# Kernel tuning notes

Measured on AMD Instinct MI355X. Metric: run time of the kernel, lower is better.

## Reference

```python
import jax, jax.numpy as jnp
import numpy as np

B, I, O = 512, 1024, 1024

def setup_inputs() -> dict:
    key = jax.random.key(0)
    kx, kw = jax.random.split(key)
    x = jax.random.normal(kx, (B, I), dtype=jnp.float32)
    W = jax.random.normal(kw, (O, I), dtype=jnp.float32)
    return {"x": x, "W": W}

def reference(x, W):
    # Tropical (max-plus) linear map: y[b, o] = max_i (x[b, i] + W[o, i])
    # Faithful to the torch broadcast-add + max-reduce formulation.
    out = x[..., None, :] + W[None, :, :]  # [B, O, I]
    return jnp.max(out, axis=-1)           # [B, O]
```

## Files before the change

### kernel.cpp

```cpp
#include <hip/hip_runtime.h>


#define B_DIM 512
#define I_DIM 1024
#define O_DIM 1024
#define BT 32
#define OT 64
#define KT 64
#define NCHUNK (I_DIM / KT)
#define XS (BT + 1)
#define WS (OT + 1)

__global__ __launch_bounds__(256, 1) void TropicalLinear_kernel(
    const float* __restrict__ x, const float* __restrict__ W,
    float* __restrict__ y)
{
    __shared__ float xs[KT * XS];
    __shared__ float ws[KT * WS];

    const int tid = threadIdx.x;
    const int to  = tid & 15;
    const int tb  = tid >> 4;
    const int b0  = blockIdx.y * BT;
    const int o0  = blockIdx.x * OT;

    const float4* xg = (const float4*)x;
    const float4* wg = (const float4*)W;

    float4 xr[2];
    float4 wr[4];

    #pragma unroll
    for (int s = 0; s < 2; ++s) {
        const int f = tid + 256 * s;
        const int r = f >> 4, c4 = f & 15;
        xr[s] = xg[(b0 + r) * (I_DIM / 4) + c4];
    }
    #pragma unroll
    for (int s = 0; s < 4; ++s) {
        const int f = tid + 256 * s;
        const int r = f >> 4, c4 = f & 15;
        wr[s] = wg[(o0 + r) * (I_DIM / 4) + c4];
    }

    float acc[2][4];
    #pragma unroll
    for (int i = 0; i < 2; ++i)
        #pragma unroll
        for (int j = 0; j < 4; ++j)
            acc[i][j] = -3.402823466e38f;

    for (int kc = 0; kc < NCHUNK; ++kc) {
        __syncthreads();

        #pragma unroll
        for (int s = 0; s < 2; ++s) {
            const int f = tid + 256 * s;
            const int r = f >> 4, c4 = f & 15;
            xs[(4 * c4 + 0) * XS + r] = xr[s].x;
            xs[(4 * c4 + 1) * XS + r] = xr[s].y;
            xs[(4 * c4 + 2) * XS + r] = xr[s].z;
            xs[(4 * c4 + 3) * XS + r] = xr[s].w;
        }
        #pragma unroll
        for (int s = 0; s < 4; ++s) {
            const int f = tid + 256 * s;
            const int r = f >> 4, c4 = f & 15;
            ws[(4 * c4 + 0) * WS + r] = wr[s].x;
            ws[(4 * c4 + 1) * WS + r] = wr[s].y;
            ws[(4 * c4 + 2) * WS + r] = wr[s].z;
            ws[(4 * c4 + 3) * WS + r] = wr[s].w;
        }
        __syncthreads();

        if (kc + 1 < NCHUNK) {
            const int k4 = (kc + 1) * (KT / 4);
            #pragma unroll
            for (int s = 0; s < 2; ++s) {
                const int f = tid + 256 * s;
                const int r = f >> 4, c4 = f & 15;
                xr[s] = xg[(b0 + r) * (I_DIM / 4) + k4 + c4];
            }
            #pragma unroll
            for (int s = 0; s < 4; ++s) {
                const int f = tid + 256 * s;
                const int r = f >> 4, c4 = f & 15;
                wr[s] = wg[(o0 + r) * (I_DIM / 4) + k4 + c4];
            }
        }

        #pragma unroll 4
        for (int k = 0; k < KT; k += 2) {
            float xa[2], xb[2];
            xa[0] = xs[k * XS + tb];
            xa[1] = xs[k * XS + tb + 16];
            xb[0] = xs[(k + 1) * XS + tb];
            xb[1] = xs[(k + 1) * XS + tb + 16];
            float w0[4], w1[4];
            #pragma unroll
            for (int j = 0; j < 4; ++j) {
                w0[j] = ws[k * WS + 4 * to + j];
                w1[j] = ws[(k + 1) * WS + 4 * to + j];
            }
            #pragma unroll
            for (int i = 0; i < 2; ++i)
                #pragma unroll
                for (int j = 0; j < 4; ++j) {
                    const float s0 = xa[i] + w0[j];
                    const float s1 = xb[i] + w1[j];
                    acc[i][j] = fmaxf(acc[i][j], fmaxf(s0, s1));
                }
        }
    }

    #pragma unroll
    for (int i = 0; i < 2; ++i) {
        float4 v = make_float4(acc[i][0], acc[i][1], acc[i][2], acc[i][3]);
        *(float4*)&y[(b0 + tb + 16 * i) * O_DIM + o0 + 4 * to] = v;
    }
}

extern "C" void kernel_launch(void* const* d_in, const int* in_sizes, int n_in,
                              void* d_out, int out_size, void* d_ws, size_t ws_size,
                              hipStream_t stream) {
    const float* x = (const float*)d_in[0];
    const float* W = (const float*)d_in[1];
    float* y = (float*)d_out;
    dim3 grid(O_DIM / OT, B_DIM / BT);
    dim3 block(256);
    TropicalLinear_kernel<<<grid, block, 0, stream>>>(x, W, y);
}
```

Measured before the change: 106.4 us.

## Use split-K 128x128 tiles with async LDS loads and atomic max reduction

Pre-transposes x and W into workspace so that K-major rows can be streamed straight into LDS with global_load_lds, double-buffered. Each thread now holds an 8x8 register tile of a 128x128 output block, which raises arithmetic per LDS read. The K dimension is split 8 ways to fill the GPU, and partial maxima are merged with int/uint atomic max/min on an output pre-filled with 0xFF. In exchange it adds two transpose launches, a memset and about four million atomics.

```diff
diff --git a/kernel.cpp b/kernel.cpp
--- a/kernel.cpp
+++ b/kernel.cpp
@@ -1,123 +1,136 @@
 #include <hip/hip_runtime.h>
+#include <float.h>
 
 
 #define B_DIM 512
 #define I_DIM 1024
 #define O_DIM 1024
-#define BT 32
-#define OT 64
-#define KT 64
-#define NCHUNK (I_DIM / KT)
-#define XS (BT + 1)
-#define WS (OT + 1)
 
-__global__ __launch_bounds__(256, 1) void TropicalLinear_kernel(
-    const float* __restrict__ x, const float* __restrict__ W,
+#define BT 128
+#define OT 128
+#define KSPLIT 8
+#define KB (I_DIM / KSPLIT)
+#define KT 32
+#define NCH (KB / KT)
+
+__device__ __forceinline__ void g2lds16(const float* g, float* l) {
+    __builtin_amdgcn_global_load_lds(
+        (const __attribute__((address_space(1))) void*)g,
+        (__attribute__((address_space(3))) void*)l, 16, 0, 0);
+}
+
+__device__ __forceinline__ void atomicMaxFloat(float* addr, float v) {
+    if (v >= 0.0f) atomicMax((int*)addr, __float_as_int(v));
+    else           atomicMin((unsigned int*)addr, __float_as_uint(v));
+}
+
+__global__ __launch_bounds__(256, 1) void trop_main(
+    const float* __restrict__ xT,
+    const float* __restrict__ wT,
     float* __restrict__ y)
 {
-    __shared__ float xs[KT * XS];
-    __shared__ float ws[KT * WS];
+    __shared__ float xs[2][KT * BT];
+    __shared__ float ws[2][KT * OT];
 
-    const int tid = threadIdx.x;
-    const int to  = tid & 15;
-    const int tb  = tid >> 4;
-    const int b0  = blockIdx.y * BT;
-    const int o0  = blockIdx.x * OT;
+    const int tid  = threadIdx.x;
+    const int to   = tid & 15;
+    const int tb   = tid >> 4;
+    const int wave = tid >> 6;
+    const int lane = tid & 63;
+    const int o0    = blockIdx.x * OT;
+    const int b0    = blockIdx.y * BT;
+    const int kbase = blockIdx.z * KB;
 
-    const float4* xg = (const float4*)x;
-    const float4* wg = (const float4*)W;
+    const int rsub = lane >> 5;
+    const int csub = (lane & 31) * 4;
 
-    float4 xr[2];
-    float4 wr[4];
+    float acc[8][8];
+    #pragma unroll
+    for (int i = 0; i < 8; ++i)
+        #pragma unroll
+        for (int j = 0; j < 8; ++j)
+            acc[i][j] = -FLT_MAX;
 
-    #pragma unroll
-    for (int s = 0; s < 2; ++s) {
-        const int f = tid + 256 * s;
-        const int r = f >> 4, c4 = f & 15;
-        xr[s] = xg[(b0 + r) * (I_DIM / 4) + c4];
-    }
-    #pragma unroll
-    for (int s = 0; s < 4; ++s) {
-        const int f = tid + 256 * s;
-        const int r = f >> 4, c4 = f & 15;
-        wr[s] = wg[(o0 + r) * (I_DIM / 4) + c4];
-    }
-
-    float acc[2][4];
-    #pragma unroll
-    for (int i = 0; i < 2; ++i)
+    auto stage = [&](int c, int buf) {
+        const int k0 = kbase + c * KT;
         #pragma unroll
-        for (int j = 0; j < 4; ++j)
-            acc[i][j] = -3.402823466e38f;
-
-    for (int kc = 0; kc < NCHUNK; ++kc) {
-        __syncthreads();
-
-        #pragma unroll
-        for (int s = 0; s < 2; ++s) {
-            const int f = tid + 256 * s;
-            const int r = f >> 4, c4 = f & 15;
-            xs[(4 * c4 + 0) * XS + r] = xr[s].x;
-            xs[(4 * c4 + 1) * XS + r] = xr[s].y;
-            xs[(4 * c4 + 2) * XS + r] = xr[s].z;
-            xs[(4 * c4 + 3) * XS + r] = xr[s].w;
+        for (int i = 0; i < 4; ++i) {
+            const int t   = wave * 4 + i;
+            const int row = k0 + 2 * t + rsub;
+            g2lds16(&xT[row * B_DIM + b0 + csub], &xs[buf][t * 256]);
         }
         #pragma unroll
-        for (int s = 0; s < 4; ++s) {
-            const int f = tid + 256 * s;
-            const int r = f >> 4, c4 = f & 15;
-            ws[(4 * c4 + 0) * WS + r] = wr[s].x;
-            ws[(4 * c4 + 1) * WS + r] = wr[s].y;
-            ws[(4 * c4 + 2) * WS + r] = wr[s].z;
-            ws[(4 * c4 + 3) * WS + r] = wr[s].w;
+        for (int i = 0; i < 4; ++i) {
+            const int t   = wave * 4 + i;
+            const int row = k0 + 2 * t + rsub;
+            g2lds16(&wT[row * O_DIM + o0 + csub], &ws[buf][t * 256]);
         }
-        __syncthreads();
+    };
 
-        if (kc + 1 < NCHUNK) {
-            const int k4 = (kc + 1) * (KT / 4);
+    auto compute = [&](int buf) {
+        for (int k = 0; k < KT; k += 2) {
+            float4 xa0 = *(const float4*)&xs[buf][k * BT + 4 * tb];
+            float4 xa1 = *(const float4*)&xs[buf][k * BT + 64 + 4 * tb];
+            float4 xb0 = *(const float4*)&xs[buf][(k + 1) * BT + 4 * tb];
+            float4 xb1 = *(const float4*)&xs[buf][(k + 1) * BT + 64 + 4 * tb];
+            float4 wa0 = *(const float4*)&ws[buf][k * OT + 4 * to];
+            float4 wa1 = *(const float4*)&ws[buf][k * OT + 64 + 4 * to];
+            float4 wb0 = *(const float4*)&ws[buf][(k + 1) * OT + 4 * to];
+            float4 wb1 = *(const float4*)&ws[buf][(k + 1) * OT + 64 + 4 * to];
+
+            const float xa[8] = {xa0.x, xa0.y, xa0.z, xa0.w, xa1.x, xa1.y, xa1.z, xa1.w};
+            const float xb[8] = {xb0.x, xb0.y, xb0.z, xb0.w, xb1.x, xb1.y, xb1.z, xb1.w};
+            const float wa[8] = {wa0.x, wa0.y, wa0.z, wa0.w, wa1.x, wa1.y, wa1.z, wa1.w};
+            const float wb[8] = {wb0.x, wb0.y, wb0.z, wb0.w, wb1.x, wb1.y, wb1.z, wb1.w};
+
             #pragma unroll
-            for (int s = 0; s < 2; ++s) {
-                const int f = tid + 256 * s;
-                const int r = f >> 4, c4 = f & 15;
-                xr[s] = xg[(b0 + r) * (I_DIM / 4) + k4 + c4];
-            }
-            #pragma unroll
-            for (int s = 0; s < 4; ++s) {
-                const int f = tid + 256 * s;
-                const int r = f >> 4, c4 = f & 15;
-                wr[s] = wg[(o0 + r) * (I_DIM / 4) + k4 + c4];
-            }
-        }
-
-        #pragma unroll 4
-        for (int k = 0; k < KT; k += 2) {
-            float xa[2], xb[2];
-            xa[0] = xs[k * XS + tb];
-            xa[1] = xs[k * XS + tb + 16];
-            xb[0] = xs[(k + 1) * XS + tb];
-            xb[1] = xs[(k + 1) * XS + tb + 16];
-            float w0[4], w1[4];
-            #pragma unroll
-            for (int j = 0; j < 4; ++j) {
-                w0[j] = ws[k * WS + 4 * to + j];
-                w1[j] = ws[(k + 1) * WS + 4 * to + j];
-            }
-            #pragma unroll
-            for (int i = 0; i < 2; ++i)
+            for (int i = 0; i < 8; ++i)
                 #pragma unroll
-                for (int j = 0; j < 4; ++j) {
-                    const float s0 = xa[i] + w0[j];
-                    const float s1 = xb[i] + w1[j];
+                for (int j = 0; j < 8; ++j) {
+                    const float s0 = xa[i] + wa[j];
+                    const float s1 = xb[i] + wb[j];
                     acc[i][j] = fmaxf(acc[i][j], fmaxf(s0, s1));
                 }
         }
+    };
+
+    stage(0, 0);
+    for (int c = 0; c < NCH; ++c) {
+        __syncthreads();
+        if (c + 1 < NCH) stage(c + 1, (c + 1) & 1);
+        compute(c & 1);
     }
 
     #pragma unroll
-    for (int i = 0; i < 2; ++i) {
-        float4 v = make_float4(acc[i][0], acc[i][1], acc[i][2], acc[i][3]);
-        *(float4*)&y[(b0 + tb + 16 * i) * O_DIM + o0 + 4 * to] = v;
-    }
+    for (int h = 0; h < 2; ++h)
+        #pragma unroll
+        for (int ii = 0; ii < 4; ++ii) {
+            const int b = b0 + 64 * h + 4 * tb + ii;
+            #pragma unroll
+            for (int g = 0; g < 2; ++g)
+                #pragma unroll
+                for (int jj = 0; jj < 4; ++jj) {
+                    const int o = o0 + 64 * g + 4 * to + jj;
+                    atomicMaxFloat(&y[b * O_DIM + o], acc[4 * h + ii][4 * g + jj]);
+                }
+        }
+}
+
+__global__ __launch_bounds__(256) void transpose_k(
+    const float* __restrict__ in, float* __restrict__ out, int R, int C)
+{
+    __shared__ float tile[32][33];
+    const int tx = threadIdx.x;
+    const int ty = threadIdx.y;
+    const int r0 = blockIdx.y * 32;
+    const int c0 = blockIdx.x * 32;
+    #pragma unroll
+    for (int i = 0; i < 4; ++i)
+        tile[ty + 8 * i][tx] = in[(r0 + ty + 8 * i) * C + c0 + tx];
+    __syncthreads();
+    #pragma unroll
+    for (int i = 0; i < 4; ++i)
+        out[(c0 + ty + 8 * i) * R + r0 + tx] = tile[tx][ty + 8 * i];
 }
 
 extern "C" void kernel_launch(void* const* d_in, const int* in_sizes, int n_in,
@@ -125,8 +138,14 @@
                               hipStream_t stream) {
     const float* x = (const float*)d_in[0];
     const float* W = (const float*)d_in[1];
-    float* y = (float*)d_out;
-    dim3 grid(O_DIM / OT, B_DIM / BT);
-    dim3 block(256);
-    TropicalLinear_kernel<<<grid, block, 0, stream>>>(x, W, y);
+    float* y  = (float*)d_out;
+    float* xT = (float*)d_ws;
+    float* wT = xT + (size_t)B_DIM * I_DIM;
+
+    transpose_k<<<dim3(I_DIM / 32, B_DIM / 32), dim3(32, 8), 0, stream>>>(x, xT, B_DIM, I_DIM);
+    transpose_k<<<dim3(I_DIM / 32, O_DIM / 32), dim3(32, 8), 0, stream>>>(W, wT, O_DIM, I_DIM);
+
+    hipMemsetAsync(d_out, 0xFF, (size_t)B_DIM * O_DIM * sizeof(float), stream);
+
+    trop_main<<<dim3(O_DIM / OT, B_DIM / BT, KSPLIT), dim3(256), 0, stream>>>(xT, wT, y);
 }
```

Result: slower. 153.1 us (+43.8%).
